# Optimization experiments

Hardware: AMD Instinct MI355X
Metric: run time of the kernel (lower is better)

Reference implementation:

```python
import jax, jax.numpy as jnp
import numpy as np

B, L, T = 4096, 1024, 32
START, STOP = T - 2, T - 1
NEG = -10000.0


def setup_inputs() -> dict:
    key = jax.random.key(0)
    k1, k2, k3 = jax.random.split(key, 3)
    feats = jax.random.normal(k1, (B, L, T), dtype=jnp.float32)
    transitions = jax.random.normal(k2, (T, T), dtype=jnp.float32)
    # CRF structural constraints from __init__: nothing transitions TO START,
    # nothing transitions FROM STOP. transitions[next, prev] convention.
    transitions = transitions.at[START, :].set(NEG).at[:, STOP].set(NEG)
    tags = jax.random.randint(k3, (B, L), 0, T - 2, dtype=jnp.int64)
    return {"feats": feats, "transitions": transitions, "tags": tags}


def reference(feats, transitions, tags):
    # feats: [B, L, T] emissions, transitions: [T, T] (next, prev), tags: [B, L]
    b, l, t = feats.shape

    # ---- forward algorithm (log partition), scan over time ----
    init = jnp.full((b, t), NEG, dtype=feats.dtype).at[:, START].set(0.0)

    def step(fv, feat_t):  # fv: [B, T] over prev tags, feat_t: [B, T]
        # tag_var[b, next, prev] = fv[b, prev] + trans[next, prev] + emit[b, next]
        tag_var = fv[:, None, :] + transitions[None, :, :] + feat_t[:, :, None]
        return jax.nn.logsumexp(tag_var, axis=2), None

    fv, _ = jax.lax.scan(step, init, jnp.swapaxes(feats, 0, 1))  # scan over L
    alpha = jax.nn.logsumexp(fv + transitions[STOP][None, :], axis=1)  # [B]

    # ---- gold path score ----
    tags_ext = jnp.concatenate(
        [jnp.full((b, 1), START, dtype=tags.dtype), tags], axis=1
    )  # [B, L+1]
    trans_score = transitions[tags_ext[:, 1:], tags_ext[:, :-1]].sum(axis=1)
    emit_score = jnp.take_along_axis(feats, tags[:, :, None], axis=2)[:, :, 0].sum(axis=1)
    gold = trans_score + emit_score + transitions[STOP, tags[:, -1]]

    return alpha - gold  # per-sequence negative log-likelihood [B]
```

## Files before the change

kernel.cpp:

```cpp
#include <hip/hip_runtime.h>
#include <hip/hip_bf16.h>


#define BATCH 4096
#define LSEQ  1024
#define T     32
#define START 30
#define STOP  31

#define LN64 4.158883083f
#define SUM_LN64 4258.6963f

typedef __attribute__((ext_vector_type(8))) short short8;
typedef __attribute__((ext_vector_type(4))) float f32x4;

static __device__ __forceinline__ short bf16b(float x) {
    union { __hip_bfloat16 h; short s; } u;
    u.h = __float2bfloat16(x);
    return u.s;
}

__global__ __launch_bounds__(64) void crf_fwd_mfma(
    const float* __restrict__ feats,
    const float* __restrict__ trans,
    const int*   __restrict__ tags,
    float*       __restrict__ out)
{
    __shared__ float trans_s[T * T];
    const int lane = threadIdx.x;
    for (int i = lane; i < T * T; i += 64) trans_s[i] = trans[i];
    __syncthreads();

    const int n = lane & 15;
    const int q = lane >> 4;
    const int b = blockIdx.x * 16 + n;

    short8 a1, a2;
    {
        const int s1 = 8 * (n >> 2) + (n & 3);
        const int s2 = s1 + 4;
#pragma unroll
        for (int j = 0; j < 8; ++j) {
            a1[j] = bf16b(__expf(trans_s[s1 * T + 8 * q + j]));
            a2[j] = bf16b(__expf(trans_s[s2 * T + 8 * q + j]));
        }
    }

    short8 bfrag;
#pragma unroll
    for (int j = 0; j < 8; ++j) bfrag[j] = 0;
    if (q == 3) bfrag[6] = bf16b(1.0f);

    const f32x4* fp = (const f32x4*)(feats + (size_t)b * (LSEQ * T) + 8 * q);
    const int*   tb = tags + (size_t)b * LSEQ;

    f32x4 fr0[8], fr1[8];
    int   tbuf[8];
#pragma unroll
    for (int i = 0; i < 8; ++i) {
        fr0[i] = fp[i * 8];
        fr1[i] = fp[i * 8 + 1];
        tbuf[i] = tb[i];
    }

    float mAcc = 0.0f;
    float gold_trans = 0.0f;
    float gold_emit  = 0.0f;
    int   prev_tag = START;
    float ev[8];
    float eCur[8];

    {
        const f32x4 g0 = fr0[0];
        const f32x4 g1 = fr1[0];
#pragma unroll
        for (int r = 0; r < 4; ++r) {
            eCur[r]     = __expf(g0[r] - LN64);
            eCur[4 + r] = __expf(g1[r] - LN64);
        }
    }

    const f32x4 zacc = {0.f, 0.f, 0.f, 0.f};

#define CRF_STEP(l, slot, DO_PF, DO_NEXT, DO_RENORM)                           \
    {                                                                          \
        const f32x4 f0  = fr0[slot];                                           \
        const f32x4 f1  = fr1[slot];                                           \
        const int   tag = tbuf[slot];                                          \
        if (DO_PF) {                                                           \
            fr0[slot]  = fp[((l) + 8) * 8];                                    \
            fr1[slot]  = fp[((l) + 8) * 8 + 1];                                \
            tbuf[slot] = tb[(l) + 8];                                          \
        }                                                                      \
        f32x4 c1 = __builtin_amdgcn_mfma_f32_16x16x32_bf16(a1, bfrag, zacc, 0, 0, 0); \
        f32x4 c2 = __builtin_amdgcn_mfma_f32_16x16x32_bf16(a2, bfrag, zacc, 0, 0, 0); \
        _Pragma("unroll")                                                      \
        for (int r = 0; r < 4; ++r) {                                          \
            ev[r]     = c1[r] * eCur[r];                                       \
            ev[4 + r] = c2[r] * eCur[4 + r];                                   \
        }                                                                      \
        _Pragma("unroll")                                                      \
        for (int j = 0; j < 8; ++j) bfrag[j] = bf16b(ev[j]);                   \
         \
        gold_trans += trans_s[tag * T + prev_tag];                             \
        {                                                                      \
            const f32x4 fs  = (tag & 4) ? f1 : f0;                             \
            const float p01 = (tag & 1) ? fs[1] : fs[0];                       \
            const float p23 = (tag & 1) ? fs[3] : fs[2];                       \
            const float pk  = (tag & 2) ? p23 : p01;                           \
            if ((tag >> 3) == q) gold_emit += pk;                              \
        }                                                                      \
        prev_tag = tag;                                                        \
        if (DO_NEXT) {  \
            const int   ns = ((slot) + 1) & 7;                                 \
            const f32x4 g0 = fr0[ns];                                          \
            const f32x4 g1 = fr1[ns];                                          \
            _Pragma("unroll")                                                  \
            for (int r = 0; r < 4; ++r) {                                      \
                eCur[r]     = __expf(g0[r] - LN64);                            \
                eCur[4 + r] = __expf(g1[r] - LN64);                            \
            }                                                                  \
        }                                                                      \
        if (DO_RENORM) {          \
            const float cb = __shfl(c1[0], n, 64);       \
            const float iv = __builtin_amdgcn_rcpf(cb);                        \
            mAcc += __logf(cb);                                                \
            _Pragma("unroll")                                                  \
            for (int j = 0; j < 8; ++j) eCur[j] *= iv;                         \
        }                                                                      \
    }

    for (int lo = 0; lo < LSEQ - 8; lo += 8) {
        CRF_STEP(lo + 0, 0, 1, 1, 0)
        CRF_STEP(lo + 1, 1, 1, 1, 0)
        CRF_STEP(lo + 2, 2, 1, 1, 0)
        CRF_STEP(lo + 3, 3, 1, 1, 0)
        CRF_STEP(lo + 4, 4, 1, 1, 0)
        CRF_STEP(lo + 5, 5, 1, 1, 0)
        CRF_STEP(lo + 6, 6, 1, 1, 0)
        CRF_STEP(lo + 7, 7, 1, 1, 1)
    }
    CRF_STEP(LSEQ - 8, 0, 0, 1, 0)
    CRF_STEP(LSEQ - 7, 1, 0, 1, 0)
    CRF_STEP(LSEQ - 6, 2, 0, 1, 0)
    CRF_STEP(LSEQ - 5, 3, 0, 1, 0)
    CRF_STEP(LSEQ - 4, 4, 0, 1, 0)
    CRF_STEP(LSEQ - 3, 5, 0, 1, 0)
    CRF_STEP(LSEQ - 2, 6, 0, 1, 0)
    CRF_STEP(LSEQ - 1, 7, 0, 0, 0)
#undef CRF_STEP

    float s = 0.0f;
#pragma unroll
    for (int j = 0; j < 8; ++j)
        s += ev[j] * __expf(trans_s[STOP * T + 8 * q + j]);
    s += __shfl_xor(s, 16, 64);
    s += __shfl_xor(s, 32, 64);
    const float alpha = mAcc + SUM_LN64 + __logf(s);

    float ge = gold_emit;
    ge += __shfl_xor(ge, 16, 64);
    ge += __shfl_xor(ge, 32, 64);
    const float gold = ge + gold_trans + trans_s[STOP * T + prev_tag];

    if (lane < 16) out[b] = alpha - gold;
}

extern "C" void kernel_launch(void* const* d_in, const int* in_sizes, int n_in,
                              void* d_out, int out_size, void* d_ws, size_t ws_size,
                              hipStream_t stream) {
    const float* feats = (const float*)d_in[0];
    const float* trans = (const float*)d_in[1];
    const int*   tags  = (const int*)d_in[2];
    float*       out   = (float*)d_out;

    crf_fwd_mfma<<<BATCH / 16, 64, 0, stream>>>(feats, trans, tags, out);
}
```

Baseline: 789.9 us.

## Move gold transition sum to separate kernel and deepen feature prefetch

Takes the gold-path transition score out of the serial MFMA recurrence and computes it in a second kernel that uses one block per sequence, with a shuffle-based parallel sum, subtracting it from the output afterwards. The prefetch ring for features and tags grows from 8 to 16 steps, and launch bounds now request one block per SM. The aim is to shorten the per-step dependency chain and hide more global-memory latency. The cost is more registers and an extra kernel launch that re-reads the tags.

```diff
diff --git a/kernel.cpp b/kernel.cpp
--- a/kernel.cpp
+++ b/kernel.cpp
@@ -13,6 +13,7 @@
 
 typedef __attribute__((ext_vector_type(8))) short short8;
 typedef __attribute__((ext_vector_type(4))) float f32x4;
+typedef __attribute__((ext_vector_type(4))) int   i32x4;
 
 static __device__ __forceinline__ short bf16b(float x) {
     union { __hip_bfloat16 h; short s; } u;
@@ -20,7 +21,7 @@
     return u.s;
 }
 
-__global__ __launch_bounds__(64) void crf_fwd_mfma(
+__global__ __launch_bounds__(64, 1) void crf_fwd_mfma(
     const float* __restrict__ feats,
     const float* __restrict__ trans,
     const int*   __restrict__ tags,
@@ -54,19 +55,17 @@
     const f32x4* fp = (const f32x4*)(feats + (size_t)b * (LSEQ * T) + 8 * q);
     const int*   tb = tags + (size_t)b * LSEQ;
 
-    f32x4 fr0[8], fr1[8];
-    int   tbuf[8];
-#pragma unroll
-    for (int i = 0; i < 8; ++i) {
+    f32x4 fr0[16], fr1[16];
+    int   tbuf[16];
+#pragma unroll
+    for (int i = 0; i < 16; ++i) {
         fr0[i] = fp[i * 8];
         fr1[i] = fp[i * 8 + 1];
         tbuf[i] = tb[i];
     }
 
     float mAcc = 0.0f;
-    float gold_trans = 0.0f;
-    float gold_emit  = 0.0f;
-    int   prev_tag = START;
+    float gold_emit = 0.0f;
     float ev[8];
     float eCur[8];
 
@@ -88,9 +87,9 @@
         const f32x4 f1  = fr1[slot];                                           \
         const int   tag = tbuf[slot];                                          \
         if (DO_PF) {                                                           \
-            fr0[slot]  = fp[((l) + 8) * 8];                                    \
-            fr1[slot]  = fp[((l) + 8) * 8 + 1];                                \
-            tbuf[slot] = tb[(l) + 8];                                          \
+            fr0[slot]  = fp[((l) + 16) * 8];                                   \
+            fr1[slot]  = fp[((l) + 16) * 8 + 1];                               \
+            tbuf[slot] = tb[(l) + 16];                                         \
         }                                                                      \
         f32x4 c1 = __builtin_amdgcn_mfma_f32_16x16x32_bf16(a1, bfrag, zacc, 0, 0, 0); \
         f32x4 c2 = __builtin_amdgcn_mfma_f32_16x16x32_bf16(a2, bfrag, zacc, 0, 0, 0); \
@@ -101,8 +100,7 @@
         }                                                                      \
         _Pragma("unroll")                                                      \
         for (int j = 0; j < 8; ++j) bfrag[j] = bf16b(ev[j]);                   \
-         \
-        gold_trans += trans_s[tag * T + prev_tag];                             \
+                            \
         {                                                                      \
             const f32x4 fs  = (tag & 4) ? f1 : f0;                             \
             const float p01 = (tag & 1) ? fs[1] : fs[0];                       \
@@ -110,9 +108,8 @@
             const float pk  = (tag & 2) ? p23 : p01;                           \
             if ((tag >> 3) == q) gold_emit += pk;                              \
         }                                                                      \
-        prev_tag = tag;                                                        \
-        if (DO_NEXT) {  \
-            const int   ns = ((slot) + 1) & 7;                                 \
+        if (DO_NEXT) { \
+            const int   ns = ((slot) + 1) & 15;                                \
             const f32x4 g0 = fr0[ns];                                          \
             const f32x4 g1 = fr1[ns];                                          \
             _Pragma("unroll")                                                  \
@@ -130,24 +127,40 @@
         }                                                                      \
     }
 
-    for (int lo = 0; lo < LSEQ - 8; lo += 8) {
-        CRF_STEP(lo + 0, 0, 1, 1, 0)
-        CRF_STEP(lo + 1, 1, 1, 1, 0)
-        CRF_STEP(lo + 2, 2, 1, 1, 0)
-        CRF_STEP(lo + 3, 3, 1, 1, 0)
-        CRF_STEP(lo + 4, 4, 1, 1, 0)
-        CRF_STEP(lo + 5, 5, 1, 1, 0)
-        CRF_STEP(lo + 6, 6, 1, 1, 0)
-        CRF_STEP(lo + 7, 7, 1, 1, 1)
-    }
-    CRF_STEP(LSEQ - 8, 0, 0, 1, 0)
-    CRF_STEP(LSEQ - 7, 1, 0, 1, 0)
-    CRF_STEP(LSEQ - 6, 2, 0, 1, 0)
-    CRF_STEP(LSEQ - 5, 3, 0, 1, 0)
-    CRF_STEP(LSEQ - 4, 4, 0, 1, 0)
-    CRF_STEP(LSEQ - 3, 5, 0, 1, 0)
-    CRF_STEP(LSEQ - 2, 6, 0, 1, 0)
-    CRF_STEP(LSEQ - 1, 7, 0, 0, 0)
+    for (int lo = 0; lo < LSEQ - 16; lo += 16) {
+        CRF_STEP(lo + 0,  0,  1, 1, 0)
+        CRF_STEP(lo + 1,  1,  1, 1, 0)
+        CRF_STEP(lo + 2,  2,  1, 1, 0)
+        CRF_STEP(lo + 3,  3,  1, 1, 0)
+        CRF_STEP(lo + 4,  4,  1, 1, 0)
+        CRF_STEP(lo + 5,  5,  1, 1, 0)
+        CRF_STEP(lo + 6,  6,  1, 1, 0)
+        CRF_STEP(lo + 7,  7,  1, 1, 1)
+        CRF_STEP(lo + 8,  8,  1, 1, 0)
+        CRF_STEP(lo + 9,  9,  1, 1, 0)
+        CRF_STEP(lo + 10, 10, 1, 1, 0)
+        CRF_STEP(lo + 11, 11, 1, 1, 0)
+        CRF_STEP(lo + 12, 12, 1, 1, 0)
+        CRF_STEP(lo + 13, 13, 1, 1, 0)
+        CRF_STEP(lo + 14, 14, 1, 1, 0)
+        CRF_STEP(lo + 15, 15, 1, 1, 1)
+    }
+    CRF_STEP(LSEQ - 16, 0,  0, 1, 0)
+    CRF_STEP(LSEQ - 15, 1,  0, 1, 0)
+    CRF_STEP(LSEQ - 14, 2,  0, 1, 0)
+    CRF_STEP(LSEQ - 13, 3,  0, 1, 0)
+    CRF_STEP(LSEQ - 12, 4,  0, 1, 0)
+    CRF_STEP(LSEQ - 11, 5,  0, 1, 0)
+    CRF_STEP(LSEQ - 10, 6,  0, 1, 0)
+    CRF_STEP(LSEQ - 9,  7,  0, 1, 1)
+    CRF_STEP(LSEQ - 8,  8,  0, 1, 0)
+    CRF_STEP(LSEQ - 7,  9,  0, 1, 0)
+    CRF_STEP(LSEQ - 6,  10, 0, 1, 0)
+    CRF_STEP(LSEQ - 5,  11, 0, 1, 0)
+    CRF_STEP(LSEQ - 4,  12, 0, 1, 0)
+    CRF_STEP(LSEQ - 3,  13, 0, 1, 0)
+    CRF_STEP(LSEQ - 2,  14, 0, 1, 0)
+    CRF_STEP(LSEQ - 1,  15, 0, 0, 0)
 #undef CRF_STEP
 
     float s = 0.0f;
@@ -161,9 +174,51 @@
     float ge = gold_emit;
     ge += __shfl_xor(ge, 16, 64);
     ge += __shfl_xor(ge, 32, 64);
-    const float gold = ge + gold_trans + trans_s[STOP * T + prev_tag];
-
-    if (lane < 16) out[b] = alpha - gold;
+
+    if (lane < 16) out[b] = alpha - ge;
+}
+
+__global__ __launch_bounds__(64) void crf_gold_trans(
+    const float* __restrict__ trans,
+    const int*   __restrict__ tags,
+    float*       __restrict__ out)
+{
+    __shared__ float trans_s[T * T];
+    const int lane = threadIdx.x;
+    for (int i = lane; i < T * T; i += 64) trans_s[i] = trans[i];
+    __syncthreads();
+
+    const int b = blockIdx.x;
+    const int* tb = tags + (size_t)b * LSEQ;
+
+    const i32x4* tp = (const i32x4*)(tb + lane * 16);
+    int tg[16];
+#pragma unroll
+    for (int v = 0; v < 4; ++v) {
+        const i32x4 t = tp[v];
+#pragma unroll
+        for (int j = 0; j < 4; ++j) tg[v * 4 + j] = t[j];
+    }
+
+    const int fromPrevLane = __shfl_up(tg[15], 1, 64);
+    int prev = (lane == 0) ? START : fromPrevLane;
+
+    float acc = 0.0f;
+#pragma unroll
+    for (int i = 0; i < 16; ++i) {
+        acc += trans_s[tg[i] * T + prev];
+        prev = tg[i];
+    }
+
+    acc += __shfl_xor(acc, 1, 64);
+    acc += __shfl_xor(acc, 2, 64);
+    acc += __shfl_xor(acc, 4, 64);
+    acc += __shfl_xor(acc, 8, 64);
+    acc += __shfl_xor(acc, 16, 64);
+    acc += __shfl_xor(acc, 32, 64);
+
+    const int lastTag = __shfl(tg[15], 63, 64);
+    if (lane == 0) out[b] -= (acc + trans_s[STOP * T + lastTag]);
 }
 
 extern "C" void kernel_launch(void* const* d_in, const int* in_sizes, int n_in,
@@ -175,4 +230,5 @@
     float*       out   = (float*)d_out;
 
     crf_fwd_mfma<<<BATCH / 16, 64, 0, stream>>>(feats, trans, tags, out);
-}
+    crf_gold_trans<<<BATCH, 64, 0, stream>>>(trans, tags, out);
+}
```

Measured after the change: 763.0 us. -3.4%, faster.
